# Performance work log

Measured on AMD Instinct MI355X. Metric: run time of the kernel, lower is better.

## Reference

```python
import jax, jax.numpy as jnp
import numpy as np

N = 100000   # nodes
E = 625000   # edges
D = 128      # input feature dim
H = 128      # hidden_channels
L = 2        # num_layers
NEG = 0.2    # leaky relu negative slope
BN_EPS = 1e-5


def setup_inputs() -> dict:
    key = jax.random.key(0)
    ks = jax.random.split(key, 12)
    s = 0.05
    return {
        "x": jax.random.normal(ks[0], (N, D), jnp.float32),
        "edge_index": jax.random.randint(ks[1], (2, E), 0, N, dtype=jnp.int32),
        "Wl": jax.random.normal(ks[2], (L, D, H), jnp.float32) * s,   # GATv2 lin_l (source)
        "bl": jax.random.normal(ks[3], (L, H), jnp.float32) * s,
        "Wr": jax.random.normal(ks[4], (L, D, H), jnp.float32) * s,   # GATv2 lin_r (target)
        "br": jax.random.normal(ks[5], (L, H), jnp.float32) * s,
        "att": jax.random.normal(ks[6], (L, H), jnp.float32) * s,     # attention vector a
        "cb": jax.random.normal(ks[7], (L, H), jnp.float32) * s,      # conv output bias
        "Wlin": jax.random.normal(ks[8], (L, H, H), jnp.float32) * s, # extra Linear
        "blin": jax.random.normal(ks[9], (L, H), jnp.float32) * s,
        "gamma": jnp.ones((L, H), jnp.float32),                       # BatchNorm weight
        "beta": jnp.zeros((L, H), jnp.float32),                       # BatchNorm bias
    }


def reference(x, edge_index, Wl, bl, Wr, br, att, cb, Wlin, blin, gamma, beta):
    src, dst = edge_index[0], edge_index[1]
    for i in range(L):
        # GATv2Conv (1 head, no self-loops)
        xs = x @ Wl[i] + bl[i]                 # [N, H] source transform
        xd = x @ Wr[i] + br[i]                 # [N, H] target transform
        e = jax.nn.leaky_relu(xs[src] + xd[dst], NEG)   # [E, H]
        logits = e @ att[i]                    # [E]
        m = jax.ops.segment_max(logits, dst, num_segments=N)
        a = jnp.exp(logits - m[dst])
        denom = jax.ops.segment_sum(a, dst, num_segments=N) + 1e-16
        alpha = a / denom[dst]                 # scatter-softmax over dst
        out = jax.ops.segment_sum(alpha[:, None] * xs[src], dst, num_segments=N) + cb[i]
        # x += lin(x)
        out = out + out @ Wlin[i] + blin[i]
        # BatchNorm1d (training mode: batch stats, biased var)
        mu = out.mean(axis=0)
        var = out.var(axis=0)
        x = (out - mu) * jax.lax.rsqrt(var + BN_EPS) * gamma[i] + beta[i]
        if i < L - 1:
            x = jax.nn.relu(x)
    return x
```

## Files before the change

### kernel.cpp

```cpp
#include <hip/hip_runtime.h>

#define NN 100000
#define NE 625000
#define HD 128

typedef unsigned int u32;
typedef unsigned short u16;
typedef __bf16 bf16x8 __attribute__((ext_vector_type(8)));
typedef float f32x4 __attribute__((ext_vector_type(4)));
typedef float f32x2 __attribute__((ext_vector_type(2)));

__device__ __forceinline__ u16 f2b(float f) {
  u32 u = __float_as_uint(f);
  u32 r = (u + 0x7FFFu + ((u >> 16) & 1u)) >> 16;
  return (u16)r;
}
__device__ __forceinline__ float b2f(u32 u) { return __uint_as_float(u << 16); }

template <int CTRL>
__device__ __forceinline__ float dppadd(float x) {
  int t = __builtin_amdgcn_update_dpp(0, __float_as_int(x), CTRL, 0xf, 0xf, true);
  return x + __int_as_float(t);
}

__global__ void k_prep_w(const float* __restrict__ Wl, const float* __restrict__ Wr,
                         const float* __restrict__ Wlin, u16* __restrict__ Wt) {
  int i = blockIdx.x * blockDim.x + threadIdx.x;
  if (i >= 6 * 16384) return;
  int mat = i >> 14;
  int l = mat / 3, which = mat % 3;
  int rem = i & 16383;
  int hh = rem >> 7, dd = rem & 127;
  const float* src = (which == 0) ? Wl : (which == 1) ? Wr : Wlin;
  float v = src[l * 16384 + dd * 128 + hh];
  if (which == 2 && dd == hh) v += 1.0f;
  Wt[l * (3 * 16384) + which * 16384 + hh * 128 + dd] = f2b(v);
}

__global__ void k_hist(const int* __restrict__ dst, int* __restrict__ deg) {
  int e = blockIdx.x * blockDim.x + threadIdx.x;
  if (e < NE) atomicAdd(&deg[dst[e]], 1);
}

__global__ void k_alloc(const int* __restrict__ deg, int* __restrict__ row_start,
                        int* __restrict__ cursor) {
  int idx = blockIdx.x * blockDim.x + threadIdx.x;
  int lane = threadIdx.x & 63;
  int v = (idx < NN) ? deg[idx] : 0;
  int incl = v;
  #pragma unroll
  for (int off = 1; off < 64; off <<= 1) {
    int t = __shfl_up(incl, off, 64);
    if (lane >= off) incl += t;
  }
  int total = __shfl(incl, 63, 64);
  int base = 0;
  if (lane == 63) base = atomicAdd(cursor, total);
  base = __shfl(base, 63, 64);
  if (idx < NN) row_start[idx] = base + incl - v;
}

__global__ void k_fill(const int* __restrict__ src, const int* __restrict__ dst,
                       const int* __restrict__ row_start, int* __restrict__ cnt,
                       int* __restrict__ ss) {
  int e = blockIdx.x * blockDim.x + threadIdx.x;
  if (e >= NE) return;
  int d = dst[e];
  int p = row_start[d] + atomicAdd(&cnt[d], 1);
  ss[p] = src[e];
}

__global__ __launch_bounds__(256) void k_gemm5(
    const u16* __restrict__ A, const float* __restrict__ A32,
    const u16* __restrict__ Bt0, const u16* __restrict__ Bt1,
    const float* __restrict__ bias0, const float* __restrict__ bias1,
    u16* __restrict__ o0, u16* __restrict__ o1,
    const float* __restrict__ bn_sum, const float* __restrict__ bn_sq,
    const float* __restrict__ bn_g, const float* __restrict__ bn_b,
    float* __restrict__ st_sum, float* __restrict__ st_sq, int nB) {
  __shared__ __align__(16) u16 lA[128 * 136];
  __shared__ __align__(16) u16 lB[64 * 136];
  const int tid = threadIdx.x;
  const int m0 = blockIdx.x * 128;
  const int rr = tid >> 4;
  const int seg = tid & 15;

  float mu[8], sc[8], bb[8];
  if (bn_sum) {
    const float invn = 1.0f / 100000.0f;
    #pragma unroll
    for (int j = 0; j < 8; ++j) {
      int c = seg * 8 + j;
      float m = bn_sum[c] * invn;
      float v = fmaxf(bn_sq[c] * invn - m * m, 0.f);
      mu[j] = m;
      sc[j] = rsqrtf(v + 1e-5f) * bn_g[c];
      bb[j] = bn_b[c];
    }
  }

  uint4 va[8];
  float4 va32a[8], va32b[8];
  #pragma unroll
  for (int p = 0; p < 8; ++p) {
    int g = m0 + p * 16 + rr;
    int gc = (g < NN) ? g : (NN - 1);
    if (A32) {
      va32a[p] = *(const float4*)(A32 + (size_t)gc * HD + seg * 8);
      va32b[p] = *(const float4*)(A32 + (size_t)gc * HD + seg * 8 + 4);
    } else {
      va[p] = *(const uint4*)(A + (size_t)gc * HD + seg * 8);
    }
  }
  uint4 vb0[4], vb1[4];
  #pragma unroll
  for (int p = 0; p < 4; ++p)
    vb0[p] = *(const uint4*)(Bt0 + (p * 16 + rr) * HD + seg * 8);
  #pragma unroll
  for (int p = 0; p < 4; ++p)
    vb1[p] = *(const uint4*)(Bt0 + (64 + p * 16 + rr) * HD + seg * 8);

  #pragma unroll
  for (int p = 0; p < 8; ++p) {
    int row = p * 16 + rr;
    uint4 v;
    if (A32) {
      float4 f0 = va32a[p], f1 = va32b[p];
      v.x = (u32)f2b(f0.x) | ((u32)f2b(f0.y) << 16);
      v.y = (u32)f2b(f0.z) | ((u32)f2b(f0.w) << 16);
      v.z = (u32)f2b(f1.x) | ((u32)f2b(f1.y) << 16);
      v.w = (u32)f2b(f1.z) | ((u32)f2b(f1.w) << 16);
    } else {
      v = va[p];
    }
    if (bn_sum) {
      u32 w[4] = {v.x, v.y, v.z, v.w};
      #pragma unroll
      for (int k = 0; k < 4; ++k) {
        float lo = fmaxf((b2f(w[k] & 0xFFFFu) - mu[2 * k]) * sc[2 * k] + bb[2 * k], 0.f);
        float hi = fmaxf((b2f(w[k] >> 16) - mu[2 * k + 1]) * sc[2 * k + 1] + bb[2 * k + 1], 0.f);
        w[k] = (u32)f2b(lo) | ((u32)f2b(hi) << 16);
      }
      v.x = w[0]; v.y = w[1]; v.z = w[2]; v.w = w[3];
    }
    *(uint4*)(lA + row * 136 + seg * 8) = v;
  }
  #pragma unroll
  for (int p = 0; p < 4; ++p)
    *(uint4*)(lB + (p * 16 + rr) * 136 + seg * 8) = vb0[p];
  __syncthreads();

  const int wv = tid >> 6;
  const int lane = tid & 63;
  const int colt = lane & 15;
  const int kq = lane >> 4;
  const int rq = kq * 4;
  bf16x8 af[2][4];
  #pragma unroll
  for (int tile = 0; tile < 2; ++tile)
    #pragma unroll
    for (int s = 0; s < 4; ++s)
      af[tile][s] = *(const bf16x8*)(lA + ((wv * 2 + tile) * 16 + colt) * 136 + s * 32 + kq * 8);

  uint4 nb0[4], nb1[4];

  for (int pass = 0; pass < nB; ++pass) {
    u16* o = pass ? o1 : o0;
    const float* bias = pass ? bias1 : bias0;
    if (pass == 1) {
      #pragma unroll
      for (int p = 0; p < 4; ++p)
        *(uint4*)(lB + (p * 16 + rr) * 136 + seg * 8) = nb0[p];
      __syncthreads();
    }
    #pragma unroll
    for (int half = 0; half < 2; ++half) {
      if (half == 1) {
        __syncthreads();
        #pragma unroll
        for (int p = 0; p < 4; ++p)
          *(uint4*)(lB + (p * 16 + rr) * 136 + seg * 8) = pass ? nb1[p] : vb1[p];
        if (pass == 0 && nB == 2) {
          #pragma unroll
          for (int p = 0; p < 4; ++p)
            nb0[p] = *(const uint4*)(Bt1 + (p * 16 + rr) * HD + seg * 8);
          #pragma unroll
          for (int p = 0; p < 4; ++p)
            nb1[p] = *(const uint4*)(Bt1 + (64 + p * 16 + rr) * HD + seg * 8);
        }
        __syncthreads();
      }
      #pragma unroll
      for (int tt = 0; tt < 4; ++tt) {
        int t = half * 4 + tt;
        bf16x8 bf[4];
        #pragma unroll
        for (int s = 0; s < 4; ++s)
          bf[s] = *(const bf16x8*)(lB + (tt * 16 + colt) * 136 + s * 32 + kq * 8);
        const int c = t * 16 + colt;
        const float bs = bias[c];
        #pragma unroll
        for (int tile = 0; tile < 2; ++tile) {
          f32x4 acc = {0.f, 0.f, 0.f, 0.f};
          #pragma unroll
          for (int s = 0; s < 4; ++s)
            acc = __builtin_amdgcn_mfma_f32_16x16x32_bf16(af[tile][s], bf[s], acc, 0, 0, 0);
          #pragma unroll
          for (int r = 0; r < 4; ++r)
            lA[((wv * 2 + tile) * 16 + rq + r) * 136 + c] = f2b(acc[r] + bs);
        }
      }
    }
    __syncthreads();
    float s8[8], q8[8];
    #pragma unroll
    for (int j = 0; j < 8; ++j) { s8[j] = 0.f; q8[j] = 0.f; }
    #pragma unroll
    for (int i = 0; i < 8; ++i) {
      int row = i * 16 + rr;
      int g = m0 + row;
      if (g < NN) {
        uint4 v = *(const uint4*)(lA + row * 136 + seg * 8);
        *(uint4*)(o + (size_t)g * HD + seg * 8) = v;
        if (st_sum && pass == 0) {
          u32 w[4] = {v.x, v.y, v.z, v.w};
          #pragma unroll
          for (int k = 0; k < 4; ++k) {
            float lo = b2f(w[k] & 0xFFFFu), hi = b2f(w[k] >> 16);
            s8[2 * k] += lo; q8[2 * k] += lo * lo;
            s8[2 * k + 1] += hi; q8[2 * k + 1] += hi * hi;
          }
        }
      }
    }
    if (st_sum && pass == 0) {
      __syncthreads();
      float* red = (float*)lB;
      #pragma unroll
      for (int j = 0; j < 8; ++j) {
        red[rr * 128 + seg * 8 + j] = s8[j];
        red[2048 + rr * 128 + seg * 8 + j] = q8[j];
      }
      __syncthreads();
      if (tid < 128) {
        float S = 0.f, Q = 0.f;
        #pragma unroll
        for (int u = 0; u < 16; ++u) {
          S += red[u * 128 + tid];
          Q += red[2048 + u * 128 + tid];
        }
        atomicAdd(&st_sum[tid], S);
        atomicAdd(&st_sq[tid], Q);
      }
    }
  }
}

__global__ __launch_bounds__(256) void k_edge4(
    const u16* __restrict__ xs_b, const u16* __restrict__ xd_b,
    const int* __restrict__ row_start, const int* __restrict__ deg,
    const int* __restrict__ ss, const float* __restrict__ att,
    const float* __restrict__ cb, u16* __restrict__ out_b) {
  int dv = blockIdx.x * 4 + (threadIdx.x >> 6);
  if (dv >= NN) return;
  const int lane = threadIdx.x & 63;
  const int cl = lane & 15;
  const int grp = lane >> 4;

  const float L2E = 1.4426950408889634f;
  float4 av0 = *(const float4*)(att + cl * 8);
  float4 av1 = *(const float4*)(att + cl * 8 + 4);
  float al[8] = {av0.x, av0.y, av0.z, av0.w, av1.x, av1.y, av1.z, av1.w};
  f32x2 a6[4], a4[4];
  #pragma unroll
  for (int k = 0; k < 4; ++k) {
    a6[k].x = L2E * 0.6f * al[2 * k];     a6[k].y = L2E * 0.6f * al[2 * k + 1];
    a4[k].x = L2E * 0.4f * al[2 * k];     a4[k].y = L2E * 0.4f * al[2 * k + 1];
  }
  uint4 xdp = *(const uint4*)(xd_b + (size_t)dv * HD + cl * 8);
  u32 xdw[4] = {xdp.x, xdp.y, xdp.z, xdp.w};
  f32x2 xd4[4];
  #pragma unroll
  for (int k = 0; k < 4; ++k) {
    xd4[k].x = __uint_as_float(xdw[k] << 16);
    xd4[k].y = __uint_as_float(xdw[k] & 0xFFFF0000u);
  }

  const int base = row_start[dv];
  const int n = deg[dv];
  f32x2 acc[4] = {{0.f, 0.f}, {0.f, 0.f}, {0.f, 0.f}, {0.f, 0.f}};
  float wsum = 0.f;

  for (int e0 = 0; e0 < n; e0 += 4) {
    int e = e0 + grp;
    int idx = ss[base + ((e < n) ? e : 0)];
    uint4 p = *(const uint4*)(xs_b + (size_t)idx * HD + cl * 8);
    u32 pw[4] = {p.x, p.y, p.z, p.w};
    f32x2 xv[4];
    f32x2 qv = {0.f, 0.f};
    #pragma unroll
    for (int k = 0; k < 4; ++k) {
      f32x2 x2;
      x2.x = __uint_as_float(pw[k] << 16);
      x2.y = __uint_as_float(pw[k] & 0xFFFF0000u);
      xv[k] = x2;
      f32x2 t = x2 + xd4[k];
      f32x2 ab = {__builtin_fabsf(t.x), __builtin_fabsf(t.y)};
      qv += a4[k] * ab;
      qv += a6[k] * t;
    }
    float q = qv.x + qv.y;
    q = dppadd<0xB1>(q);
    q = dppadd<0x4E>(q);
    q = dppadd<0x124>(q);
    q = dppadd<0x128>(q);
    float w = (e < n) ? exp2f(q) : 0.f;
    wsum += w;
    #pragma unroll
    for (int k = 0; k < 4; ++k) acc[k] += xv[k] * w;
  }

  #pragma unroll
  for (int k = 0; k < 4; ++k) {
    acc[k].x += __shfl_xor(acc[k].x, 16, 64);
    acc[k].y += __shfl_xor(acc[k].y, 16, 64);
    acc[k].x += __shfl_xor(acc[k].x, 32, 64);
    acc[k].y += __shfl_xor(acc[k].y, 32, 64);
  }
  wsum += __shfl_xor(wsum, 16, 64);
  wsum += __shfl_xor(wsum, 32, 64);

  if (grp == 0) {
    float inv = 1.f / (wsum + 1e-16f);
    float4 cb0 = *(const float4*)(cb + cl * 8);
    float4 cb1 = *(const float4*)(cb + cl * 8 + 4);
    float cbl[8] = {cb0.x, cb0.y, cb0.z, cb0.w, cb1.x, cb1.y, cb1.z, cb1.w};
    u32 ow[4];
    #pragma unroll
    for (int k = 0; k < 4; ++k) {
      float o0 = acc[k].x * inv + cbl[2 * k];
      float o1 = acc[k].y * inv + cbl[2 * k + 1];
      ow[k] = (u32)f2b(o0) | ((u32)f2b(o1) << 16);
    }
    uint4 o;
    o.x = ow[0]; o.y = ow[1]; o.z = ow[2]; o.w = ow[3];
    *(uint4*)(out_b + (size_t)dv * HD + cl * 8) = o;
  }
}

__global__ void k_bn(const u16* __restrict__ hb, const float* __restrict__ ssum,
                     const float* __restrict__ ssq, const float* __restrict__ gamma,
                     const float* __restrict__ beta, float* __restrict__ fout) {
  int i = blockIdx.x * blockDim.x + threadIdx.x;
  if (i >= NN * 64) return;
  int cp = (i & 63) * 2;
  u32 xp = ((const u32*)hb)[i];
  float v0 = b2f(xp & 0xFFFFu), v1 = b2f(xp >> 16);
  const float invn = 1.0f / 100000.0f;
  float mu0 = ssum[cp] * invn, mu1 = ssum[cp + 1] * invn;
  float va0 = fmaxf(ssq[cp] * invn - mu0 * mu0, 0.f);
  float va1 = fmaxf(ssq[cp + 1] * invn - mu1 * mu1, 0.f);
  float s0 = rsqrtf(va0 + 1e-5f) * gamma[cp];
  float s1 = rsqrtf(va1 + 1e-5f) * gamma[cp + 1];
  float o0 = (v0 - mu0) * s0 + beta[cp];
  float o1 = (v1 - mu1) * s1 + beta[cp + 1];
  int row = i >> 6;
  *(float2*)(fout + row * 128 + cp) = make_float2(o0, o1);
}

extern "C" void kernel_launch(void* const* d_in, const int* in_sizes, int n_in,
                              void* d_out, int out_size, void* d_ws, size_t ws_size,
                              hipStream_t stream) {
  const float* x    = (const float*)d_in[0];
  const int*   ei   = (const int*)d_in[1];
  const float* Wl   = (const float*)d_in[2];
  const float* bl   = (const float*)d_in[3];
  const float* Wr   = (const float*)d_in[4];
  const float* br   = (const float*)d_in[5];
  const float* att  = (const float*)d_in[6];
  const float* cb   = (const float*)d_in[7];
  const float* Wlin = (const float*)d_in[8];
  const float* blin = (const float*)d_in[9];
  const float* gm   = (const float*)d_in[10];
  const float* bt   = (const float*)d_in[11];
  const int* esrc = ei;
  const int* edst = ei + NE;

  u16* xs_b  = (u16*)d_ws;
  u16* xd_b  = xs_b + NN * HD;
  u16* out_b = xd_b + NN * HD;
  u16* Wt    = out_b + NN * HD;
  int* deg       = (int*)(Wt + 6 * 16384);
  int* cnt       = deg + NN;
  int* cursor    = cnt + NN;
  int* row_start = cursor + 1;
  int* srcs      = row_start + NN;
  float* ssum0   = (float*)(srcs + NE);
  float* ssq0    = ssum0 + 128;
  float* ssum1   = ssq0 + 128;
  float* ssq1    = ssum1 + 128;

  hipMemsetAsync(deg, 0, (size_t)(2 * NN + 1) * 4, stream);
  hipMemsetAsync(ssum0, 0, 4 * 128 * 4, stream);
  k_prep_w<<<(6 * 16384 + 255) / 256, 256, 0, stream>>>(Wl, Wr, Wlin, Wt);
  k_hist<<<(NE + 255) / 256, 256, 0, stream>>>(edst, deg);
  k_alloc<<<(NN + 255) / 256, 256, 0, stream>>>(deg, row_start, cursor);
  k_fill<<<(NE + 255) / 256, 256, 0, stream>>>(esrc, edst, row_start, cnt, srcs);

  const int gg = (NN + 127) / 128;
  const u16* wt0_l = Wt;             const u16* wt0_r = Wt + 16384;     const u16* wt0_lin = Wt + 2 * 16384;
  const u16* wt1_l = Wt + 3 * 16384; const u16* wt1_r = Wt + 4 * 16384; const u16* wt1_lin = Wt + 5 * 16384;

  k_gemm5<<<gg, 256, 0, stream>>>(nullptr, x, wt0_l, wt0_r, bl, br, xs_b, xd_b,
                                  nullptr, nullptr, nullptr, nullptr,
                                  nullptr, nullptr, 2);
  k_edge4<<<(NN + 3) / 4, 256, 0, stream>>>(xs_b, xd_b, row_start, deg, srcs,
                                            att, cb, out_b);
  k_gemm5<<<gg, 256, 0, stream>>>(out_b, nullptr, wt0_lin, nullptr, blin, nullptr,
                                  out_b, nullptr,
                                  nullptr, nullptr, nullptr, nullptr,
                                  ssum0, ssq0, 1);
  k_gemm5<<<gg, 256, 0, stream>>>(out_b, nullptr, wt1_l, wt1_r, bl + 128, br + 128,
                                  xs_b, xd_b,
                                  ssum0, ssq0, gm, bt,
                                  nullptr, nullptr, 2);
  k_edge4<<<(NN + 3) / 4, 256, 0, stream>>>(xs_b, xd_b, row_start, deg, srcs,
                                            att + 128, cb + 128, out_b);
  k_gemm5<<<gg, 256, 0, stream>>>(out_b, nullptr, wt1_lin, nullptr, blin + 128, nullptr,
                                  out_b, nullptr,
                                  nullptr, nullptr, nullptr, nullptr,
                                  ssum1, ssq1, 1);
  k_bn<<<(NN * 64 + 255) / 256, 256, 0, stream>>>(out_b, ssum1, ssq1,
                                                  gm + 128, bt + 128, (float*)d_out);
}
```

Before: 474.2 us.

## Halve GEMM row tile, pre-cast x to bf16, merge init kernels

The GEMM now handles 64 rows per block instead of 128, with launch bounds of 4 blocks per CU, so it uses less LDS and fewer registers and can keep more blocks resident. It also no longer carries the fp32 input path; x is instead cast to bf16 ahead of time inside a new fused init kernel. That init kernel also does the weight transpose and the degree histogram, which saves launches. In exchange, x is read in fp32 once and then written and re-read as bf16, weight tiles are reloaded by twice as many blocks, and the second weight load is deferred to after the first sync.

Result: slower. 537.4 us (+13.3%).

```diff
diff --git a/kernel.cpp b/kernel.cpp
--- a/kernel.cpp
+++ b/kernel.cpp
@@ -3,6 +3,8 @@
 #define NN 100000
 #define NE 625000
 #define HD 128
+#define CAST_N (NN * 32)
+#define PREP_N (6 * 16384)
 
 typedef unsigned int u32;
 typedef unsigned short u16;
@@ -23,23 +25,31 @@
   return x + __int_as_float(t);
 }
 
-__global__ void k_prep_w(const float* __restrict__ Wl, const float* __restrict__ Wr,
-                         const float* __restrict__ Wlin, u16* __restrict__ Wt) {
+__global__ void k_init(const float* __restrict__ x, u16* __restrict__ xb,
+                       const float* __restrict__ Wl, const float* __restrict__ Wr,
+                       const float* __restrict__ Wlin, u16* __restrict__ Wt,
+                       const int* __restrict__ dst, int* __restrict__ deg) {
   int i = blockIdx.x * blockDim.x + threadIdx.x;
-  if (i >= 6 * 16384) return;
-  int mat = i >> 14;
-  int l = mat / 3, which = mat % 3;
-  int rem = i & 16383;
-  int hh = rem >> 7, dd = rem & 127;
-  const float* src = (which == 0) ? Wl : (which == 1) ? Wr : Wlin;
-  float v = src[l * 16384 + dd * 128 + hh];
-  if (which == 2 && dd == hh) v += 1.0f;
-  Wt[l * (3 * 16384) + which * 16384 + hh * 128 + dd] = f2b(v);
-}
-
-__global__ void k_hist(const int* __restrict__ dst, int* __restrict__ deg) {
-  int e = blockIdx.x * blockDim.x + threadIdx.x;
-  if (e < NE) atomicAdd(&deg[dst[e]], 1);
+  if (i < CAST_N) {
+    float4 v = *(const float4*)(x + (size_t)i * 4);
+    uint2 o;
+    o.x = (u32)f2b(v.x) | ((u32)f2b(v.y) << 16);
+    o.y = (u32)f2b(v.z) | ((u32)f2b(v.w) << 16);
+    *(uint2*)(xb + (size_t)i * 4) = o;
+  } else if (i < CAST_N + PREP_N) {
+    int j = i - CAST_N;
+    int mat = j >> 14;
+    int l = mat / 3, which = mat % 3;
+    int rem = j & 16383;
+    int hh = rem >> 7, dd = rem & 127;
+    const float* src = (which == 0) ? Wl : (which == 1) ? Wr : Wlin;
+    float v = src[l * 16384 + dd * 128 + hh];
+    if (which == 2 && dd == hh) v += 1.0f;
+    Wt[l * (3 * 16384) + which * 16384 + hh * 128 + dd] = f2b(v);
+  } else {
+    int e = i - CAST_N - PREP_N;
+    if (e < NE) atomicAdd(&deg[dst[e]], 1);
+  }
 }
 
 __global__ void k_alloc(const int* __restrict__ deg, int* __restrict__ row_start,
@@ -70,18 +80,17 @@
   ss[p] = src[e];
 }
 
-__global__ __launch_bounds__(256) void k_gemm5(
-    const u16* __restrict__ A, const float* __restrict__ A32,
-    const u16* __restrict__ Bt0, const u16* __restrict__ Bt1,
+__global__ __launch_bounds__(256, 4) void k_gemm6(
+    const u16* __restrict__ A, const u16* __restrict__ Bt0, const u16* __restrict__ Bt1,
     const float* __restrict__ bias0, const float* __restrict__ bias1,
     u16* __restrict__ o0, u16* __restrict__ o1,
     const float* __restrict__ bn_sum, const float* __restrict__ bn_sq,
     const float* __restrict__ bn_g, const float* __restrict__ bn_b,
     float* __restrict__ st_sum, float* __restrict__ st_sq, int nB) {
-  __shared__ __align__(16) u16 lA[128 * 136];
+  __shared__ __align__(16) u16 lA[64 * 136];
   __shared__ __align__(16) u16 lB[64 * 136];
   const int tid = threadIdx.x;
-  const int m0 = blockIdx.x * 128;
+  const int m0 = blockIdx.x * 64;
   const int rr = tid >> 4;
   const int seg = tid & 15;
 
@@ -99,40 +108,22 @@
     }
   }
 
-  uint4 va[8];
-  float4 va32a[8], va32b[8];
-  #pragma unroll
-  for (int p = 0; p < 8; ++p) {
+  uint4 va[4];
+  #pragma unroll
+  for (int p = 0; p < 4; ++p) {
     int g = m0 + p * 16 + rr;
     int gc = (g < NN) ? g : (NN - 1);
-    if (A32) {
-      va32a[p] = *(const float4*)(A32 + (size_t)gc * HD + seg * 8);
-      va32b[p] = *(const float4*)(A32 + (size_t)gc * HD + seg * 8 + 4);
-    } else {
-      va[p] = *(const uint4*)(A + (size_t)gc * HD + seg * 8);
-    }
-  }
-  uint4 vb0[4], vb1[4];
+    va[p] = *(const uint4*)(A + (size_t)gc * HD + seg * 8);
+  }
+  uint4 vb0[4];
   #pragma unroll
   for (int p = 0; p < 4; ++p)
     vb0[p] = *(const uint4*)(Bt0 + (p * 16 + rr) * HD + seg * 8);
-  #pragma unroll
-  for (int p = 0; p < 4; ++p)
-    vb1[p] = *(const uint4*)(Bt0 + (64 + p * 16 + rr) * HD + seg * 8);
-
-  #pragma unroll
-  for (int p = 0; p < 8; ++p) {
+
+  #pragma unroll
+  for (int p = 0; p < 4; ++p) {
     int row = p * 16 + rr;
-    uint4 v;
-    if (A32) {
-      float4 f0 = va32a[p], f1 = va32b[p];
-      v.x = (u32)f2b(f0.x) | ((u32)f2b(f0.y) << 16);
-      v.y = (u32)f2b(f0.z) | ((u32)f2b(f0.w) << 16);
-      v.z = (u32)f2b(f1.x) | ((u32)f2b(f1.y) << 16);
-      v.w = (u32)f2b(f1.z) | ((u32)f2b(f1.w) << 16);
-    } else {
-      v = va[p];
-    }
+    uint4 v = va[p];
     if (bn_sum) {
       u32 w[4] = {v.x, v.y, v.z, v.w};
       #pragma unroll
@@ -150,17 +141,20 @@
     *(uint4*)(lB + (p * 16 + rr) * 136 + seg * 8) = vb0[p];
   __syncthreads();
 
+  uint4 vb1[4];
+  #pragma unroll
+  for (int p = 0; p < 4; ++p)
+    vb1[p] = *(const uint4*)(Bt0 + (64 + p * 16 + rr) * HD + seg * 8);
+
   const int wv = tid >> 6;
   const int lane = tid & 63;
   const int colt = lane & 15;
   const int kq = lane >> 4;
   const int rq = kq * 4;
-  bf16x8 af[2][4];
-  #pragma unroll
-  for (int tile = 0; tile < 2; ++tile)
-    #pragma unroll
-    for (int s = 0; s < 4; ++s)
-      af[tile][s] = *(const bf16x8*)(lA + ((wv * 2 + tile) * 16 + colt) * 136 + s * 32 + kq * 8);
+  bf16x8 af[4];
+  #pragma unroll
+  for (int s = 0; s < 4; ++s)
+    af[s] = *(const bf16x8*)(lA + (wv * 16 + colt) * 136 + s * 32 + kq * 8);
 
   uint4 nb0[4], nb1[4];
 
@@ -199,16 +193,13 @@
           bf[s] = *(const bf16x8*)(lB + (tt * 16 + colt) * 136 + s * 32 + kq * 8);
         const int c = t * 16 + colt;
         const float bs = bias[c];
+        f32x4 acc = {0.f, 0.f, 0.f, 0.f};
         #pragma unroll
-        for (int tile = 0; tile < 2; ++tile) {
-          f32x4 acc = {0.f, 0.f, 0.f, 0.f};
-          #pragma unroll
-          for (int s = 0; s < 4; ++s)
-            acc = __builtin_amdgcn_mfma_f32_16x16x32_bf16(af[tile][s], bf[s], acc, 0, 0, 0);
-          #pragma unroll
-          for (int r = 0; r < 4; ++r)
-            lA[((wv * 2 + tile) * 16 + rq + r) * 136 + c] = f2b(acc[r] + bs);
-        }
+        for (int s = 0; s < 4; ++s)
+          acc = __builtin_amdgcn_mfma_f32_16x16x32_bf16(af[s], bf[s], acc, 0, 0, 0);
+        #pragma unroll
+        for (int r = 0; r < 4; ++r)
+          lA[(wv * 16 + rq + r) * 136 + c] = f2b(acc[r] + bs);
       }
     }
     __syncthreads();
@@ -216,7 +207,7 @@
     #pragma unroll
     for (int j = 0; j < 8; ++j) { s8[j] = 0.f; q8[j] = 0.f; }
     #pragma unroll
-    for (int i = 0; i < 8; ++i) {
+    for (int i = 0; i < 4; ++i) {
       int row = i * 16 + rr;
       int g = m0 + row;
       if (g < NN) {
@@ -386,7 +377,8 @@
   const int* esrc = ei;
   const int* edst = ei + NE;
 
-  u16* xs_b  = (u16*)d_ws;
+  u16* xb    = (u16*)d_ws;
+  u16* xs_b  = xb + NN * HD;
   u16* xd_b  = xs_b + NN * HD;
   u16* out_b = xd_b + NN * HD;
   u16* Wt    = out_b + NN * HD;
@@ -402,31 +394,31 @@
 
   hipMemsetAsync(deg, 0, (size_t)(2 * NN + 1) * 4, stream);
   hipMemsetAsync(ssum0, 0, 4 * 128 * 4, stream);
-  k_prep_w<<<(6 * 16384 + 255) / 256, 256, 0, stream>>>(Wl, Wr, Wlin, Wt);
-  k_hist<<<(NE + 255) / 256, 256, 0, stream>>>(edst, deg);
+  k_init<<<(CAST_N + PREP_N + NE + 255) / 256, 256, 0, stream>>>(
+      x, xb, Wl, Wr, Wlin, Wt, edst, deg);
   k_alloc<<<(NN + 255) / 256, 256, 0, stream>>>(deg, row_start, cursor);
   k_fill<<<(NE + 255) / 256, 256, 0, stream>>>(esrc, edst, row_start, cnt, srcs);
 
-  const int gg = (NN + 127) / 128;
+  const int gg = (NN + 63) / 64;
   const u16* wt0_l = Wt;             const u16* wt0_r = Wt + 16384;     const u16* wt0_lin = Wt + 2 * 16384;
   const u16* wt1_l = Wt + 3 * 16384; const u16* wt1_r = Wt + 4 * 16384; const u16* wt1_lin = Wt + 5 * 16384;
 
-  k_gemm5<<<gg, 256, 0, stream>>>(nullptr, x, wt0_l, wt0_r, bl, br, xs_b, xd_b,
+  k_gemm6<<<gg, 256, 0, stream>>>(xb, wt0_l, wt0_r, bl, br, xs_b, xd_b,
                                   nullptr, nullptr, nullptr, nullptr,
                                   nullptr, nullptr, 2);
   k_edge4<<<(NN + 3) / 4, 256, 0, stream>>>(xs_b, xd_b, row_start, deg, srcs,
                                             att, cb, out_b);
-  k_gemm5<<<gg, 256, 0, stream>>>(out_b, nullptr, wt0_lin, nullptr, blin, nullptr,
+  k_gemm6<<<gg, 256, 0, stream>>>(out_b, wt0_lin, nullptr, blin, nullptr,
                                   out_b, nullptr,
                                   nullptr, nullptr, nullptr, nullptr,
                                   ssum0, ssq0, 1);
-  k_gemm5<<<gg, 256, 0, stream>>>(out_b, nullptr, wt1_l, wt1_r, bl + 128, br + 128,
+  k_gemm6<<<gg, 256, 0, stream>>>(out_b, wt1_l, wt1_r, bl + 128, br + 128,
                                   xs_b, xd_b,
                                   ssum0, ssq0, gm, bt,
                                   nullptr, nullptr, 2);
   k_edge4<<<(NN + 3) / 4, 256, 0, stream>>>(xs_b, xd_b, row_start, deg, srcs,
                                             att + 128, cb + 128, out_b);
-  k_gemm5<<<gg, 256, 0, stream>>>(out_b, nullptr, wt1_lin, nullptr, blin + 128, nullptr,
+  k_gemm6<<<gg, 256, 0, stream>>>(out_b, wt1_lin, nullptr, blin + 128, nullptr,
                                   out_b, nullptr,
                                   nullptr, nullptr, nullptr, nullptr,
                                   ssum1, ssq1, 1);
```
